# Performance work log

Measured on AMD Instinct MI355X. Metric: run time of the kernel, lower is better.

Reference implementation:

```python
import jax, jax.numpy as jnp
import numpy as np

N_DIMS = 256
HW = 32
FILTERS = [32, 64, 128, 256]
SCALES = [16, 8, 4, 2]
B = 4


def _ds(t, s):
    # Exact bilinear downsample (align_corners=False, half-pixel centers) by even integer factor s:
    # target coord (i+0.5)*s - 0.5 = s*i + s/2 - 0.5 -> mean of neighbours s*i+s//2-1 and s*i+s//2.
    if s == 1:
        return t
    oH, oW = t.shape[2] // s, t.shape[3] // s
    ih = jnp.arange(oH) * s + s // 2 - 1
    iw = jnp.arange(oW) * s + s // 2 - 1
    t = 0.5 * (t[:, :, ih, :] + t[:, :, ih + 1, :])
    t = 0.5 * (t[:, :, :, iw] + t[:, :, :, iw + 1])
    return t


def _spp(t, s, w, scale, bias):
    # Upsample(1/s) -> Conv3x3(no bias) -> BN(folded to scale/bias, eval form) -> ReLU
    t = _ds(t, s)
    t = jax.lax.conv_general_dilated(t, w, (1, 1), 'SAME',
                                     dimension_numbers=('NCHW', 'OIHW', 'NCHW'))
    return jax.nn.relu(t * scale[None, :, None, None] + bias[None, :, None, None])


def setup_inputs() -> dict:
    key = jax.random.key(0)
    ks = iter(jax.random.split(key, 32))
    d = {}
    d['x'] = jax.random.normal(next(ks), (B, N_DIMS, HW, HW), jnp.float32)
    sizes = [HW * s for s in SCALES]
    for i, (c, sz) in enumerate(zip(FILTERS, sizes)):
        d[f'x{i}'] = jax.random.normal(next(ks), (B, c, sz, sz), jnp.float32)
    for i, c in enumerate(FILTERS):
        d[f'w{i}'] = jax.random.normal(next(ks), (N_DIMS, c, 3, 3), jnp.float32) * (1.0 / np.sqrt(9 * c))
        d[f's{i}'] = jax.random.normal(next(ks), (N_DIMS,), jnp.float32) * 0.1 + 1.0
        d[f'b{i}'] = jax.random.normal(next(ks), (N_DIMS,), jnp.float32) * 0.1
    dq = N_DIMS // 8
    d['qw'] = jax.random.normal(next(ks), (dq, N_DIMS), jnp.float32) * (1.0 / np.sqrt(N_DIMS))
    d['qb'] = jnp.zeros((dq,), jnp.float32)
    d['kw'] = jax.random.normal(next(ks), (dq, N_DIMS), jnp.float32) * (1.0 / np.sqrt(N_DIMS))
    d['kb'] = jnp.zeros((dq,), jnp.float32)
    d['vw'] = jax.random.normal(next(ks), (N_DIMS, N_DIMS), jnp.float32) * (1.0 / np.sqrt(N_DIMS))
    d['vb'] = jnp.zeros((N_DIMS,), jnp.float32)
    d['rel_h'] = jax.random.normal(next(ks), (1, dq, HW, 1), jnp.float32)
    d['rel_w'] = jax.random.normal(next(ks), (1, dq, 1, HW), jnp.float32)
    d['gamma'] = jax.random.normal(next(ks), (1,), jnp.float32) * 0.5  # torch inits to 0; nonzero for useful test
    return d


def reference(x, x0, x1, x2, x3,
              w0, s0, b0, w1, s1, b1, w2, s2, b2, w3, s3, b3,
              qw, qb, kw, kb, vw, vb, rel_h, rel_w, gamma):
    Bm, C, H, W = x.shape
    N = H * W
    multi_x = (_spp(x0, 16, w0, s0, b0) + _spp(x1, 8, w1, s1, b1)
               + _spp(x2, 4, w2, s2, b2) + _spp(x3, 2, w3, s3, b3))
    # 1x1 convs as channel matmuls
    q = jnp.einsum('bchw,oc->bohw', multi_x, qw) + qb[None, :, None, None]
    k = jnp.einsum('bchw,oc->bohw', x, kw) + kb[None, :, None, None]
    v = jnp.einsum('bchw,oc->bohw', x, vw) + vb[None, :, None, None]
    q = q.reshape(Bm, -1, N).transpose(0, 2, 1)          # [B, N, C/8]
    k = k.reshape(Bm, -1, N)                             # [B, C/8, N]
    v = v.reshape(Bm, C, N)                              # [B, C, N]
    energy = jnp.einsum('bnc,bcm->bnm', q, k)            # content
    pos = (rel_h + rel_w).reshape(C // 8, N)             # [C/8, N]
    energy = energy + jnp.einsum('bnc,cm->bnm', q, pos)  # + position bias
    attn = jax.nn.softmax(energy, axis=-1)               # [B, N, N]
    out = jnp.einsum('bcj,bij->bci', v, attn).reshape(Bm, C, H, W)
    out = gamma * out + x
    return out, attn
```

## Files before the change

kernel.cpp:

```cpp
#include <hip/hip_runtime.h>
#include <stdint.h>

#define BN 4
#define CC 256
#define DQ 32
#define HWD 32
#define NN 1024

typedef __attribute__((ext_vector_type(8))) short short8v;
typedef __attribute__((ext_vector_type(16))) float float16v;

#define W3OFF0 0
#define W3OFF1 73728
#define W3OFF2 221184
#define W3OFF3 516096
#define WQOFF  1105920
#define WKOFF  1114112
#define WVOFF  1122304
#define WPKTOT 1187840

#define PREP_PAD 8880
#define PREP_RPK 4640
#define PREP_XT  512
#define PREP_TOT (PREP_PAD + PREP_RPK + PREP_XT)

#define CP_PROJ 288
#define CP_CONV 1024
#define CP_TOT  (CP_PROJ + CP_CONV)

#define LDS_STRIDE 7872

__device__ __forceinline__ short f2bf(float f) {
  union { float f; uint32_t u; } v; v.f = f;
  uint32_t r = v.u + 0x7FFFu + ((v.u >> 16) & 1u);
  return (short)(r >> 16);
}

__device__ __forceinline__ void gl_lds16(const short* g, short* l) {
  __builtin_amdgcn_global_load_lds(
      (const __attribute__((address_space(1))) void*)g,
      (__attribute__((address_space(3))) void*)l, 16, 0, 0);
}

__global__ __launch_bounds__(256) void prep_kernel(
    const float* __restrict__ x0, const float* __restrict__ x1,
    const float* __restrict__ x2, const float* __restrict__ x3,
    const float* __restrict__ w0, const float* __restrict__ w1,
    const float* __restrict__ w2, const float* __restrict__ w3,
    const float* __restrict__ qw, const float* __restrict__ kw,
    const float* __restrict__ vw, const float* __restrict__ x,
    short* __restrict__ pim, short* __restrict__ wpk,
    short* __restrict__ xT2) {
  __shared__ float t[64][33];
  int bid = blockIdx.x;
  int tid = threadIdx.x;
  if (bid < PREP_PAD) {
    int plane = bid / 37;
    int idx = (bid % 37) * 256 + tid;
    if (idx >= 9248) return;
    int b = plane / 60, g = plane % 60;
    int pr = idx / 272;
    int rem = idx % 272;
    int pc = rem >> 3, j = rem & 7;
    const float* xs;
    int s, gb, C;
    if (g < 4)       { xs = x0; s = 16; gb = 0;  C = 32; }
    else if (g < 12) { xs = x1; s = 8;  gb = 4;  C = 64; }
    else if (g < 28) { xs = x2; s = 4;  gb = 12; C = 128; }
    else             { xs = x3; s = 2;  gb = 28; C = 256; }
    float v = 0.f;
    if (pr >= 1 && pr <= 32 && pc >= 1 && pc <= 32) {
      int c = (g - gb) * 8 + j;
      int inHW = 32 * s;
      int ih = (pr - 1) * s + (s >> 1) - 1;
      int iw = (pc - 1) * s + (s >> 1) - 1;
      const float* p = xs + ((size_t)(b * C + c) * inHW + ih) * inHW + iw;
      v = 0.25f * (p[0] + p[1] + p[inHW] + p[inHW + 1]);
    }
    pim[(size_t)plane * 9248 + idx] = f2bf(v);
  } else if (bid < PREP_PAD + PREP_RPK) {
    int idx = (bid - PREP_PAD) * 256 + tid;
    if (idx >= WPKTOT) return;
    const float* w;
    int Cin, chunks, taps, ridx;
    if (idx < W3OFF1)      { w = w0; Cin = 32;  chunks = 2;  taps = 9; ridx = idx; }
    else if (idx < W3OFF2) { w = w1; Cin = 64;  chunks = 4;  taps = 9; ridx = idx - W3OFF1; }
    else if (idx < W3OFF3) { w = w2; Cin = 128; chunks = 8;  taps = 9; ridx = idx - W3OFF2; }
    else if (idx < WQOFF)  { w = w3; Cin = 256; chunks = 16; taps = 9; ridx = idx - W3OFF3; }
    else if (idx < WKOFF)  { w = qw; Cin = 256; chunks = 16; taps = 1; ridx = idx - WQOFF; }
    else if (idx < WVOFF)  { w = kw; Cin = 256; chunks = 16; taps = 1; ridx = idx - WKOFF; }
    else                   { w = vw; Cin = 256; chunks = 16; taps = 1; ridx = idx - WVOFF; }
    int per = taps * 512;
    int g2 = ridx / per;
    int rem = ridx % per;
    int tap = rem >> 9;
    int l = (rem >> 3) & 63;
    int j = rem & 7;
    int ocg = g2 / chunks;
    int chunk = g2 % chunks;
    int oc = ocg * 32 + (l & 31);
    int c = chunk * 16 + ((l >> 5) << 3) + j;
    wpk[idx] = f2bf(w[((size_t)oc * Cin + c) * taps + tap]);
  } else {
    int xb = bid - PREP_PAD - PREP_RPK;
    int nb = xb & 31;
    int cb = (xb >> 5) & 3;
    int b = xb >> 7;
    int n0 = nb * 32, c0 = cb * 64;
    int a = tid >> 5, e = tid & 31;
#pragma unroll
    for (int k = 0; k < 8; ++k)
      t[a + 8 * k][e] = x[((size_t)(b * CC + c0 + a + 8 * k) * NN) + n0 + e];
    __syncthreads();
    int n = tid & 31, cg = tid >> 5;
    short8v o;
#pragma unroll
    for (int jj = 0; jj < 8; ++jj) o[jj] = f2bf(t[cg * 8 + jj][n]);
    *(short8v*)(xT2 + (((size_t)(b * 32) + cb * 8 + cg) * 1024 + n0 + n) * 8) = o;
  }
}

template<int CHUNKS, int GB, int WOFS_>
__device__ __forceinline__ void conv_body_lds(
    const short* __restrict__ pim, const short* __restrict__ wpk,
    const float* __restrict__ sc, const float* __restrict__ bi,
    short* __restrict__ multiT4, short* lds,
    int b, int ocg, int rowq, int sp) {
  int tid = threadIdx.x;
  int w = tid >> 6, l = tid & 63;
  int col = l & 31, chH = l >> 5;
  int r0 = rowq * 4;
  int oc0 = ocg * 32;
  const short* asrc0 = wpk + WOFS_ + (size_t)(ocg * CHUNKS) * 4608;

  auto STAGE = [&](int ck, int buf) {
    short* A = lds + buf * LDS_STRIDE;
    short* B = A + 4608;
    const short* as = asrc0 + (size_t)ck * 4608;
    const short* p0 = pim + ((size_t)(b * 60 + GB + 2 * ck) * 1156 + r0 * 34) * 8;
    const short* p1 = pim + ((size_t)(b * 60 + GB + 2 * ck + 1) * 1156 + r0 * 34) * 8;
    gl_lds16(as + tid * 8, A + (size_t)w * 512);
    gl_lds16(as + (tid + 256) * 8, A + 2048 + (size_t)w * 512);
    if (w == 0) gl_lds16(as + (tid + 512) * 8, A + 4096);
    if (tid < 204) {
      gl_lds16(p0 + tid * 8, B + (size_t)w * 512);
      gl_lds16(p1 + tid * 8, B + 1632 + (size_t)w * 512);
    }
  };

  float16v acc;
#pragma unroll
  for (int r = 0; r < 16; ++r) acc[r] = 0.f;

  STAGE(0, 0);
  __syncthreads();
  int cur = 0;
#pragma unroll
  for (int ck = 0; ck < CHUNKS; ++ck) {
    if (ck + 1 < CHUNKS) STAGE(ck + 1, cur ^ 1);
    const short* A = lds + cur * LDS_STRIDE;
    const short* B = A + 4608;
#pragma unroll
    for (int ky = 0; ky < 3; ++ky)
#pragma unroll
      for (int kx = 0; kx < 3; ++kx) {
        short8v av = *(const short8v*)&A[(ky * 3 + kx) * 512 + l * 8];
        short8v bv = *(const short8v*)&B[chH * 1632 + (w + ky) * 272 + (col + kx) * 8];
        acc = __builtin_amdgcn_mfma_f32_32x32x16_bf16(av, bv, acc, 0, 0, 0);
      }
    __syncthreads();
    cur ^= 1;
  }

  float* sTw = ((float*)lds) + w * (32 * 33);
#pragma unroll
  for (int r = 0; r < 16; ++r) {
    int ocl = (r & 3) + ((r >> 2) << 3) + (chH << 2);
    float t = fmaf(acc[r], sc[oc0 + ocl], bi[oc0 + ocl]);
    sTw[ocl * 33 + col] = t > 0.f ? t : 0.f;
  }
  __syncthreads();
#pragma unroll
  for (int it = 0; it < 2; ++it) {
    int idx = l + (it << 6);
    int cg = idx >> 5;
    int c2 = idx & 31;
    short8v o;
#pragma unroll
    for (int jj = 0; jj < 8; ++jj) o[jj] = f2bf(sTw[(cg * 8 + jj) * 33 + c2]);
    *(short8v*)(multiT4 + (size_t)sp * 1048576 +
                (((size_t)(b * 32) + ocg * 4 + cg) * 1024 + (r0 + w) * 32 + c2) * 8) = o;
  }
}

__global__ __launch_bounds__(256) void convproj2_kernel(
    const short* __restrict__ pim, const short* __restrict__ wpk,
    const short* __restrict__ xT2,
    const float* __restrict__ sc0, const float* __restrict__ bi0,
    const float* __restrict__ sc1, const float* __restrict__ bi1,
    const float* __restrict__ sc2, const float* __restrict__ bi2,
    const float* __restrict__ sc3, const float* __restrict__ bi3,
    const float* __restrict__ kbi, const float* __restrict__ vbi,
    const float* __restrict__ relh, const float* __restrict__ relw,
    short* __restrict__ multiT4, float* __restrict__ kpbuf,
    short* __restrict__ vbf2) {
  __shared__ short lds[2 * LDS_STRIDE];
  int bid = blockIdx.x;
  int tid = threadIdx.x;
  if (bid < CP_PROJ) {
    int u = bid * 4 + (tid >> 6);
    int l = tid & 63;
    int mode, b, nt, ocg;
    const short* ap;
    const float* bias;
    if (u < 128) { mode = 1; b = u >> 5; nt = u & 31; ocg = 0; ap = wpk + WKOFF; bias = kbi; }
    else { int t2 = u - 128; mode = 2; nt = t2 & 31; ocg = (t2 >> 5) & 7; b = t2 >> 8; ap = wpk + WVOFF + (size_t)ocg * 16 * 512; bias = vbi; }
    int n = nt * 32 + (l & 31);
    int half = l >> 5;
    ap += l * 8;
    float16v acc;
#pragma unroll
    for (int r = 0; r < 16; ++r) acc[r] = 0.f;
#pragma unroll
    for (int ck = 0; ck < 16; ++ck) {
      short8v av = *(const short8v*)(ap + ck * 512);
      short8v bv = *(const short8v*)(xT2 + (((size_t)(b * 32) + ck * 2 + half) * 1024 + n) * 8);
      acc = __builtin_amdgcn_mfma_f32_32x32x16_bf16(av, bv, acc, 0, 0, 0);
    }
#pragma unroll
    for (int r = 0; r < 16; ++r) {
      int oc = ocg * 32 + (r & 3) + ((r >> 2) << 3) + (half << 2);
      float t = acc[r] + bias[oc];
      if (mode == 1) {
        t += relh[oc * 32 + (n >> 5)] + relw[oc * 32 + (n & 31)];
        kpbuf[((size_t)b * DQ + oc) * NN + n] = t;
      } else {
        vbf2[(((size_t)(b * 128) + (n >> 3)) * 256 + oc) * 8 + (n & 7)] = f2bf(t);
      }
    }
  } else {
    int cb = bid - CP_PROJ;
    int s = cb & 3;
    int rowq = (cb >> 2) & 7;
    int ocg = (cb >> 5) & 7;
    int b = cb >> 8;
    if (s == 0)      conv_body_lds<2, 0, W3OFF0>(pim, wpk, sc0, bi0, multiT4, lds, b, ocg, rowq, 0);
    else if (s == 1) conv_body_lds<4, 4, W3OFF1>(pim, wpk, sc1, bi1, multiT4, lds, b, ocg, rowq, 1);
    else if (s == 2) conv_body_lds<8, 12, W3OFF2>(pim, wpk, sc2, bi2, multiT4, lds, b, ocg, rowq, 2);
    else             conv_body_lds<16, 28, W3OFF3>(pim, wpk, sc3, bi3, multiT4, lds, b, ocg, rowq, 3);
  }
}

__global__ __launch_bounds__(256) void attn2_kernel(
    const short* __restrict__ multiT4, const short* __restrict__ wpk,
    const float* __restrict__ qbi, const float* __restrict__ kp,
    float* __restrict__ attn, short* __restrict__ abf2) {
  __shared__ float lds_q[4][32][33];
  __shared__ float qs[DQ][8];
  __shared__ float redm[4][8], reds[4][8];
  int bidx = blockIdx.x;
  int ig = bidx & 127;
  int b = bidx >> 7;
  int i0 = ig * 8;
  int tid = threadIdx.x;
  int w = tid >> 6, l = tid & 63;
  int it0 = (ig >> 2) * 32;

  {
    int n = it0 + (l & 31);
    int half = l >> 5;
    const short* ap = wpk + WQOFF + l * 8;
    float16v acc;
#pragma unroll
    for (int r = 0; r < 16; ++r) acc[r] = 0.f;
#pragma unroll
    for (int c4 = 0; c4 < 4; ++c4) {
      int ck = w * 4 + c4;
      short8v av = *(const short8v*)(ap + ck * 512);
      size_t bix = (((size_t)(b * 32) + ck * 2 + half) * 1024 + n) * 8;
      short8v bv0 = *(const short8v*)(multiT4 + bix);
      short8v bv1 = *(const short8v*)(multiT4 + 1048576 + bix);
      short8v bv2 = *(const short8v*)(multiT4 + 2097152 + bix);
      short8v bv3 = *(const short8v*)(multiT4 + 3145728 + bix);
      acc = __builtin_amdgcn_mfma_f32_32x32x16_bf16(av, bv0, acc, 0, 0, 0);
      acc = __builtin_amdgcn_mfma_f32_32x32x16_bf16(av, bv1, acc, 0, 0, 0);
      acc = __builtin_amdgcn_mfma_f32_32x32x16_bf16(av, bv2, acc, 0, 0, 0);
      acc = __builtin_amdgcn_mfma_f32_32x32x16_bf16(av, bv3, acc, 0, 0, 0);
    }
#pragma unroll
    for (int r = 0; r < 16; ++r) {
      int oc = (r & 3) + ((r >> 2) << 3) + (half << 2);
      lds_q[w][oc][l & 31] = acc[r];
    }
  }
  __syncthreads();
  {
    int c = tid >> 3, rr = tid & 7;
    int nl = (ig & 3) * 8 + rr;
    qs[c][rr] = lds_q[0][c][nl] + lds_q[1][c][nl] + lds_q[2][c][nl] +
                lds_q[3][c][nl] + qbi[c];
  }
  __syncthreads();

  float e[8][4];
#pragma unroll
  for (int r = 0; r < 8; ++r)
#pragma unroll
    for (int k = 0; k < 4; ++k) e[r][k] = 0.f;
  const float* kpb = kp + (size_t)b * DQ * NN + tid;
  for (int c = 0; c < DQ; ++c) {
    float k0 = kpb[0], k1 = kpb[256], k2 = kpb[512], k3 = kpb[768];
    kpb += NN;
#pragma unroll
    for (int r = 0; r < 8; ++r) {
      float qv = qs[c][r];
      e[r][0] = fmaf(qv, k0, e[r][0]);
      e[r][1] = fmaf(qv, k1, e[r][1]);
      e[r][2] = fmaf(qv, k2, e[r][2]);
      e[r][3] = fmaf(qv, k3, e[r][3]);
    }
  }
  int lane = tid & 63, wvi = tid >> 6;
#pragma unroll
  for (int r = 0; r < 8; ++r) {
    float mm = fmaxf(fmaxf(e[r][0], e[r][1]), fmaxf(e[r][2], e[r][3]));
#pragma unroll
    for (int off = 32; off > 0; off >>= 1) mm = fmaxf(mm, __shfl_xor(mm, off));
    if (lane == 0) redm[wvi][r] = mm;
  }
  __syncthreads();
#pragma unroll
  for (int r = 0; r < 8; ++r) {
    float mm = fmaxf(fmaxf(redm[0][r], redm[1][r]), fmaxf(redm[2][r], redm[3][r]));
    float ss = 0.f;
#pragma unroll
    for (int k = 0; k < 4; ++k) {
      e[r][k] = __expf(e[r][k] - mm);
      ss += e[r][k];
    }
#pragma unroll
    for (int off = 32; off > 0; off >>= 1) ss += __shfl_xor(ss, off);
    if (lane == 0) reds[wvi][r] = ss;
  }
  __syncthreads();
#pragma unroll
  for (int r = 0; r < 8; ++r) {
    float inv = 1.f / (reds[0][r] + reds[1][r] + reds[2][r] + reds[3][r]);
    int i = i0 + r;
    size_t base = ((size_t)b * NN + i) * NN + tid;
#pragma unroll
    for (int k = 0; k < 4; ++k) {
      int j = tid + k * 256;
      float a = e[r][k] * inv;
      attn[base + k * 256] = a;
      abf2[(((size_t)(b * 128) + (j >> 3)) * 1024 + i) * 8 + (j & 7)] = f2bf(a);
    }
  }
}

__global__ __launch_bounds__(256) void out_mfma2_kernel(
    const short* __restrict__ vbf2, const short* __restrict__ abf2,
    const float* __restrict__ x, const float* __restrict__ gamma,
    float* __restrict__ out) {
  int tid = threadIdx.x;
  int l = tid & 63;
  int wv = tid >> 6;
  int wc = wv >> 1, wi = wv & 1;
  int bid = blockIdx.x;
  int ig = bid & 15;
  int cg = (bid >> 4) & 3;
  int b = bid >> 6;
  int c0 = cg * 64 + wc * 32;
  int i0 = ig * 64 + wi * 32;
  int half = l >> 5, lane31 = l & 31;

  const short* vbase = vbf2 + (size_t)b * 128 * 256 * 8 + ((size_t)half * 256 + c0 + lane31) * 8;
  const short* abase = abf2 + (size_t)b * 128 * 1024 * 8 + ((size_t)half * 1024 + i0 + lane31) * 8;

  float16v acc;
#pragma unroll
  for (int r = 0; r < 16; ++r) acc[r] = 0.f;

#pragma unroll 4
  for (int jc = 0; jc < 128; jc += 2) {
    short8v av = *(const short8v*)(vbase + (size_t)jc * 256 * 8);
    short8v bv = *(const short8v*)(abase + (size_t)jc * 1024 * 8);
    acc = __builtin_amdgcn_mfma_f32_32x32x16_bf16(av, bv, acc, 0, 0, 0);
  }

  float g = gamma[0];
  int i = i0 + lane31;
#pragma unroll
  for (int r = 0; r < 16; ++r) {
    int c = c0 + (r & 3) + ((r >> 2) << 3) + (half << 2);
    size_t off = ((size_t)b * CC + c) * NN + i;
    out[off] = fmaf(g, acc[r], x[off]);
  }
}

extern "C" void kernel_launch(void* const* d_in, const int* in_sizes, int n_in,
                              void* d_out, int out_size, void* d_ws, size_t ws_size,
                              hipStream_t stream) {
  const float* x    = (const float*)d_in[0];
  const float* x0   = (const float*)d_in[1];
  const float* x1   = (const float*)d_in[2];
  const float* x2   = (const float*)d_in[3];
  const float* x3   = (const float*)d_in[4];
  const float* w0   = (const float*)d_in[5];
  const float* s0   = (const float*)d_in[6];
  const float* b0   = (const float*)d_in[7];
  const float* w1   = (const float*)d_in[8];
  const float* s1   = (const float*)d_in[9];
  const float* b1   = (const float*)d_in[10];
  const float* w2   = (const float*)d_in[11];
  const float* s2   = (const float*)d_in[12];
  const float* b2   = (const float*)d_in[13];
  const float* w3   = (const float*)d_in[14];
  const float* s3   = (const float*)d_in[15];
  const float* b3   = (const float*)d_in[16];
  const float* qw   = (const float*)d_in[17];
  const float* qbi  = (const float*)d_in[18];
  const float* kw   = (const float*)d_in[19];
  const float* kbi  = (const float*)d_in[20];
  const float* vw   = (const float*)d_in[21];
  const float* vbi  = (const float*)d_in[22];
  const float* relh = (const float*)d_in[23];
  const float* relw = (const float*)d_in[24];
  const float* gamma= (const float*)d_in[25];

  float* ws = (float*)d_ws;
  short* pim     = (short*)ws;
  short* multiT4 = (short*)(ws + 1109760);
  float* kpbuf   = ws + 3337984;
  short* xT2     = (short*)(ws + 3469056);
  short* vbf2    = (short*)(ws + 3993344);
  short* wpk     = (short*)(ws + 4517632);
  short* abf2    = (short*)(ws + 5111552);

  float* out  = (float*)d_out;
  float* attn = out + (size_t)BN * CC * NN;

  prep_kernel<<<PREP_TOT, 256, 0, stream>>>(x0, x1, x2, x3, w0, w1, w2, w3,
                                            qw, kw, vw, x, pim, wpk, xT2);

  convproj2_kernel<<<CP_TOT, 256, 0, stream>>>(pim, wpk, xT2,
                                               s0, b0, s1, b1, s2, b2, s3, b3,
                                               kbi, vbi, relh, relw,
                                               multiT4, kpbuf, vbf2);

  attn2_kernel<<<512, 256, 0, stream>>>(multiT4, wpk, qbi, kpbuf, attn, abf2);

  out_mfma2_kernel<<<256, 256, 0, stream>>>(vbf2, abf2, x, gamma, out);
}
```

Measured before the change: 89.19 us.

## Fuse attention softmax and output matmul, keeping probabilities in LDS

Merges the attention kernel and the attn·V output kernel into one. Each block converts its 8 rows of softmax probabilities to bf16 in shared memory (unioned with the q scratch) and immediately multiplies them against V with MFMA, writing the residual output. This removes the global bf16 attention buffer round trip and a kernel launch. In exchange, every block rereads all of V and wastes most of each 32-wide MFMA tile since only 8 query rows are valid.

New measurement: 89.14 us. No clear change (-0.1%).

```diff
diff --git a/kernel.cpp b/kernel.cpp
--- a/kernel.cpp
+++ b/kernel.cpp
@@ -29,6 +29,7 @@
 #define CP_TOT  (CP_PROJ + CP_CONV)
 
 #define LDS_STRIDE 7872
+#define PROWS 1032
 
 __device__ __forceinline__ short f2bf(float f) {
   union { float f; uint32_t u; } v; v.f = f;
@@ -251,11 +252,16 @@
   }
 }
 
-__global__ __launch_bounds__(256) void attn2_kernel(
+__global__ __launch_bounds__(256) void attnout_kernel(
     const short* __restrict__ multiT4, const short* __restrict__ wpk,
     const float* __restrict__ qbi, const float* __restrict__ kp,
-    float* __restrict__ attn, short* __restrict__ abf2) {
-  __shared__ float lds_q[4][32][33];
+    const short* __restrict__ vbf2, const float* __restrict__ x,
+    const float* __restrict__ gamma, float* __restrict__ attn,
+    float* __restrict__ out) {
+  __shared__ union {
+    float lds_q[4][32][33];
+    short P[8][PROWS];
+  } u;
   __shared__ float qs[DQ][8];
   __shared__ float redm[4][8], reds[4][8];
   int bidx = blockIdx.x;
@@ -290,15 +296,15 @@
 #pragma unroll
     for (int r = 0; r < 16; ++r) {
       int oc = (r & 3) + ((r >> 2) << 3) + (half << 2);
-      lds_q[w][oc][l & 31] = acc[r];
+      u.lds_q[w][oc][l & 31] = acc[r];
     }
   }
   __syncthreads();
   {
     int c = tid >> 3, rr = tid & 7;
     int nl = (ig & 3) * 8 + rr;
-    qs[c][rr] = lds_q[0][c][nl] + lds_q[1][c][nl] + lds_q[2][c][nl] +
-                lds_q[3][c][nl] + qbi[c];
+    qs[c][rr] = u.lds_q[0][c][nl] + u.lds_q[1][c][nl] + u.lds_q[2][c][nl] +
+                u.lds_q[3][c][nl] + qbi[c];
   }
   __syncthreads();
 
@@ -350,51 +356,40 @@
     size_t base = ((size_t)b * NN + i) * NN + tid;
 #pragma unroll
     for (int k = 0; k < 4; ++k) {
-      int j = tid + k * 256;
-      float a = e[r][k] * inv;
-      attn[base + k * 256] = a;
-      abf2[(((size_t)(b * 128) + (j >> 3)) * 1024 + i) * 8 + (j & 7)] = f2bf(a);
-    }
-  }
-}
-
-__global__ __launch_bounds__(256) void out_mfma2_kernel(
-    const short* __restrict__ vbf2, const short* __restrict__ abf2,
-    const float* __restrict__ x, const float* __restrict__ gamma,
-    float* __restrict__ out) {
-  int tid = threadIdx.x;
-  int l = tid & 63;
-  int wv = tid >> 6;
-  int wc = wv >> 1, wi = wv & 1;
-  int bid = blockIdx.x;
-  int ig = bid & 15;
-  int cg = (bid >> 4) & 3;
-  int b = bid >> 6;
-  int c0 = cg * 64 + wc * 32;
-  int i0 = ig * 64 + wi * 32;
-  int half = l >> 5, lane31 = l & 31;
-
-  const short* vbase = vbf2 + (size_t)b * 128 * 256 * 8 + ((size_t)half * 256 + c0 + lane31) * 8;
-  const short* abase = abf2 + (size_t)b * 128 * 1024 * 8 + ((size_t)half * 1024 + i0 + lane31) * 8;
-
-  float16v acc;
-#pragma unroll
-  for (int r = 0; r < 16; ++r) acc[r] = 0.f;
-
+      float av = e[r][k] * inv;
+      attn[base + k * 256] = av;
+      u.P[r][tid + k * 256] = f2bf(av);
+    }
+  }
+  __syncthreads();
+
+  {
+    int half = l >> 5, lane31 = l & 31;
+    float g = gamma[0];
+    const short* prow = &u.P[lane31 & 7][half * 8];
+#pragma unroll
+    for (int ct = 0; ct < 2; ++ct) {
+      int c0 = (w * 2 + ct) * 32;
+      const short* vbase = vbf2 + (((size_t)(b * 128) + half) * 256 + c0 + lane31) * 8;
+      float16v acc;
+#pragma unroll
+      for (int r = 0; r < 16; ++r) acc[r] = 0.f;
 #pragma unroll 4
-  for (int jc = 0; jc < 128; jc += 2) {
-    short8v av = *(const short8v*)(vbase + (size_t)jc * 256 * 8);
-    short8v bv = *(const short8v*)(abase + (size_t)jc * 1024 * 8);
-    acc = __builtin_amdgcn_mfma_f32_32x32x16_bf16(av, bv, acc, 0, 0, 0);
-  }
-
-  float g = gamma[0];
-  int i = i0 + lane31;
-#pragma unroll
-  for (int r = 0; r < 16; ++r) {
-    int c = c0 + (r & 3) + ((r >> 2) << 3) + (half << 2);
-    size_t off = ((size_t)b * CC + c) * NN + i;
-    out[off] = fmaf(g, acc[r], x[off]);
+      for (int jc = 0; jc < 64; ++jc) {
+        short8v av = *(const short8v*)(vbase + (size_t)jc * 2 * 256 * 8);
+        short8v bv = *(const short8v*)(prow + jc * 16);
+        acc = __builtin_amdgcn_mfma_f32_32x32x16_bf16(av, bv, acc, 0, 0, 0);
+      }
+      if (lane31 < 8) {
+        int i = i0 + lane31;
+#pragma unroll
+        for (int r = 0; r < 16; ++r) {
+          int c = c0 + (r & 3) + ((r >> 2) << 3) + (half << 2);
+          size_t off = ((size_t)b * CC + c) * NN + i;
+          out[off] = fmaf(g, acc[r], x[off]);
+        }
+      }
+    }
   }
 }
 
@@ -435,7 +430,6 @@
   short* xT2     = (short*)(ws + 3469056);
   short* vbf2    = (short*)(ws + 3993344);
   short* wpk     = (short*)(ws + 4517632);
-  short* abf2    = (short*)(ws + 5111552);
 
   float* out  = (float*)d_out;
   float* attn = out + (size_t)BN * CC * NN;
@@ -448,7 +442,6 @@
                                                kbi, vbi, relh, relw,
                                                multiT4, kpbuf, vbf2);
 
-  attn2_kernel<<<512, 256, 0, stream>>>(multiT4, wpk, qbi, kpbuf, attn, abf2);
-
-  out_mfma2_kernel<<<256, 256, 0, stream>>>(vbf2, abf2, x, gamma, out);
-}
+  attnout_kernel<<<512, 256, 0, stream>>>(multiT4, wpk, qbi, kpbuf,
+                                          vbf2, x, gamma, attn, out);
+}
```
